# Optimization experiments

Hardware: AMD Instinct MI355X
Metric: run time of the kernel (lower is better)

Reference implementation:

```python
import jax, jax.numpy as jnp
import numpy as np

B, S, E, H = 2, 2048, 1024, 16
HD = E // H


def setup_inputs() -> dict:
    key = jax.random.key(0)
    ks = jax.random.split(key, 5)
    scale = 1.0 / np.sqrt(E)
    return {
        "x": jax.random.normal(ks[0], (B, S, E), dtype=jnp.float32),
        "Wq": jax.random.normal(ks[1], (H, HD, E), dtype=jnp.float32) * scale,
        "Wk": jax.random.normal(ks[2], (H, HD, E), dtype=jnp.float32) * scale,
        "Wv": jax.random.normal(ks[3], (H, HD, E), dtype=jnp.float32) * scale,
        "Wo": jax.random.normal(ks[4], (E, E), dtype=jnp.float32) * scale,
    }


def reference(x, Wq, Wk, Wv, Wo):
    # Batched per-head projections: torch Linear y = x @ W.T, W: [head_dim, E]
    q = jnp.einsum("bse,hde->bshd", x, Wq)  # [B,S,H,HD]
    k = jnp.einsum("bse,hde->bshd", x, Wk)
    v = jnp.einsum("bse,hde->bshd", x, Wv)
    # Scaled dot-product attention; original scales by sqrt(head_dim)
    scores = jnp.einsum("bqhd,bkhd->bhqk", q, k) / jnp.sqrt(jnp.float32(HD))
    attn = jax.nn.softmax(scores, axis=-1)  # [B,H,S,S]
    out_h = jnp.einsum("bhqk,bkhd->bqhd", attn, v)  # [B,S,H,HD]
    out_cat = out_h.reshape(x.shape[0], x.shape[1], -1)  # concat heads -> [B,S,E]
    return out_cat @ Wo.T
```

## Files before the change

### kernel.cpp

```cpp
#include <hip/hip_runtime.h>
#include <hip/hip_bf16.h>

typedef unsigned short u16;
typedef unsigned int u32;
typedef __attribute__((ext_vector_type(4))) float f32x4;
typedef __attribute__((ext_vector_type(16))) float f32x16;
typedef __attribute__((ext_vector_type(8))) short short8;
typedef __attribute__((ext_vector_type(8))) unsigned short u16x8;
typedef __attribute__((ext_vector_type(4))) unsigned short u16x4;
typedef __attribute__((ext_vector_type(4))) unsigned int u32x4;

#define BATCH 2
#define SEQ   2048
#define EMB   1024
#define NH    16
#define HD    64

__device__ inline u16 f2bf(float f) {
    unsigned u = __builtin_bit_cast(unsigned, f);
    unsigned r = u + 0x7FFFu + ((u >> 16) & 1u);
    return (u16)(r >> 16);
}

__device__ inline float fexp2(float x) {
    float r;
    asm("v_exp_f32 %0, %1" : "=v"(r) : "v"(x));
    return r;
}

__device__ inline void gload16(const void* g, void* l) {
    __builtin_amdgcn_global_load_lds(
        (const __attribute__((address_space(1))) unsigned int*)g,
        (__attribute__((address_space(3))) unsigned int*)l, 16, 0, 0);
}

__device__ inline short8 mk8(u32 a, u32 b, u32 c, u32 d) {
    u32x4 t; t[0] = a; t[1] = b; t[2] = c; t[3] = d;
    return __builtin_bit_cast(short8, t);
}

#define PACK_ST(st, w0,w1,w2,w3,w4,w5,w6,w7)                                   \
  {                                                                            \
    asm("v_cvt_pk_bf16_f32 %0, %1, %2" : "=v"(w0) : "v"(st[0]),  "v"(st[1]));  \
    asm("v_cvt_pk_bf16_f32 %0, %1, %2" : "=v"(w1) : "v"(st[2]),  "v"(st[3]));  \
    asm("v_cvt_pk_bf16_f32 %0, %1, %2" : "=v"(w2) : "v"(st[4]),  "v"(st[5]));  \
    asm("v_cvt_pk_bf16_f32 %0, %1, %2" : "=v"(w3) : "v"(st[6]),  "v"(st[7]));  \
    asm("v_permlane32_swap_b32 %0, %1" : "+v"(w0), "+v"(w2));                  \
    asm("v_permlane32_swap_b32 %0, %1" : "+v"(w1), "+v"(w3));                  \
    asm("v_cvt_pk_bf16_f32 %0, %1, %2" : "=v"(w4) : "v"(st[8]),  "v"(st[9]));  \
    asm("v_cvt_pk_bf16_f32 %0, %1, %2" : "=v"(w5) : "v"(st[10]), "v"(st[11])); \
    asm("v_cvt_pk_bf16_f32 %0, %1, %2" : "=v"(w6) : "v"(st[12]), "v"(st[13])); \
    asm("v_cvt_pk_bf16_f32 %0, %1, %2" : "=v"(w7) : "v"(st[14]), "v"(st[15])); \
    asm("v_permlane32_swap_b32 %0, %1" : "+v"(w4), "+v"(w6));                  \
    asm("v_permlane32_swap_b32 %0, %1" : "+v"(w5), "+v"(w7));                  \
  }

__global__ __launch_bounds__(256) void convert_all(
    const float* __restrict__ x,
    const float* __restrict__ Wq, const float* __restrict__ Wk, const float* __restrict__ Wv,
    u16* __restrict__ Xb, u16* __restrict__ Wqkv)
{
    const long gidx = (long)blockIdx.x * 2048 + (long)threadIdx.x * 8;
    const float* src;
    u16* dst;
    if (gidx < 4194304L) {
        src = x + gidx; dst = Xb + gidx;
    } else {
        const long r = gidx - 4194304L;
        const int w = (int)(r >> 20);
        const long off = r & 1048575L;
        src = (w == 0 ? Wq : w == 1 ? Wk : Wv) + off;
        dst = Wqkv + r;
    }
    f32x4 a = *(const f32x4*)src;
    f32x4 b = *(const f32x4*)(src + 4);
    u16x8 o;
    #pragma unroll
    for (int j = 0; j < 4; ++j) { o[j] = f2bf(a[j]); o[4 + j] = f2bf(b[j]); }
    *(u16x8*)dst = o;
}

__global__ __launch_bounds__(256) void convert_wo(
    const float* __restrict__ Wo, u16* __restrict__ Wob)
{
    const long gidx = (long)blockIdx.x * 2048 + (long)threadIdx.x * 8;
    f32x4 a = *(const f32x4*)(Wo + gidx);
    f32x4 b = *(const f32x4*)(Wo + gidx + 4);
    u16x8 o;
    #pragma unroll
    for (int j = 0; j < 4; ++j) { o[j] = f2bf(a[j]); o[4 + j] = f2bf(b[j]); }
    *(u16x8*)(Wob + gidx) = o;
}

__global__ __launch_bounds__(512, 2) void gemm256(
    const u16* __restrict__ A, const u16* __restrict__ Bb,
    u16* __restrict__ Qo, u16* __restrict__ Ko, u16* __restrict__ VTo)
{
    __shared__ u16 As[2][256 * 64];
    __shared__ u16 Bs[2][192 * 64];

    const int tid = threadIdx.x;
    const int lane = tid & 63;
    const int wid = tid >> 6;
    const int lr = lane & 15;
    const int lg = lane >> 4;
    const int wr = wid >> 2;
    const int wc = wid & 3;

    const int lin = blockIdx.y * 16 + blockIdx.x;
    const int swz = (lin & 7) * 32 + (lin >> 3);
    const int m0 = (swz & 15) * 256;
    const int n0 = (swz >> 4) * 192;

    const int grow = lane >> 3;
    const int schunk = ((lane & 7) ^ grow) << 4;

    auto issueTile = [&](int kt, int buf) {
        const int k0b = kt * 128;
        #pragma unroll
        for (int i = 0; i < 4; ++i) {
            const int row = i * 64 + wid * 8 + grow;
            gload16((const char*)A + (size_t)(m0 + row) * 2048 + k0b + schunk,
                    (char*)As[buf] + i * 8192 + wid * 1024);
        }
        #pragma unroll
        for (int i = 0; i < 3; ++i) {
            const int row = i * 64 + wid * 8 + grow;
            gload16((const char*)Bb + (size_t)(n0 + row) * 2048 + k0b + schunk,
                    (char*)Bs[buf] + i * 8192 + wid * 1024);
        }
    };

    issueTile(0, 0);
    issueTile(1, 1);

    f32x4 acc[8][3] = {};
    const int rsw = (lr & 7);

    for (int t = 0; t < 16; ++t) {
        if (t < 15) { asm volatile("s_waitcnt vmcnt(7)" ::: "memory"); }
        else        { asm volatile("s_waitcnt vmcnt(0)" ::: "memory"); }
        __builtin_amdgcn_sched_barrier(0);
        __builtin_amdgcn_s_barrier();
        __builtin_amdgcn_sched_barrier(0);

        const u16* Ac = As[t & 1];
        const u16* Bc = Bs[t & 1];

        short8 a[4][2], b[3][2];

        #pragma unroll
        for (int fi = 0; fi < 4; ++fi)
            #pragma unroll
            for (int ks = 0; ks < 2; ++ks)
                a[fi][ks] = *(const short8*)((const char*)Ac + (wr * 128 + fi * 16 + lr) * 128
                                             + (((ks * 4 + lg) ^ rsw) << 4));
        #pragma unroll
        for (int fj = 0; fj < 3; ++fj)
            #pragma unroll
            for (int ks = 0; ks < 2; ++ks)
                b[fj][ks] = *(const short8*)((const char*)Bc + (wc * 48 + fj * 16 + lr) * 128
                                             + (((ks * 4 + lg) ^ rsw) << 4));
        __builtin_amdgcn_s_setprio(1);
        #pragma unroll
        for (int fi = 0; fi < 4; ++fi)
            #pragma unroll
            for (int fj = 0; fj < 3; ++fj)
                #pragma unroll
                for (int ks = 0; ks < 2; ++ks)
                    acc[fi][fj] = __builtin_amdgcn_mfma_f32_16x16x32_bf16(a[fi][ks], b[fj][ks], acc[fi][fj], 0, 0, 0);
        __builtin_amdgcn_s_setprio(0);

        #pragma unroll
        for (int fi = 0; fi < 4; ++fi)
            #pragma unroll
            for (int ks = 0; ks < 2; ++ks)
                a[fi][ks] = *(const short8*)((const char*)Ac + (wr * 128 + (fi + 4) * 16 + lr) * 128
                                             + (((ks * 4 + lg) ^ rsw) << 4));
        __builtin_amdgcn_s_setprio(1);
        #pragma unroll
        for (int fi = 0; fi < 4; ++fi)
            #pragma unroll
            for (int fj = 0; fj < 3; ++fj)
                #pragma unroll
                for (int ks = 0; ks < 2; ++ks)
                    acc[fi + 4][fj] = __builtin_amdgcn_mfma_f32_16x16x32_bf16(a[fi][ks], b[fj][ks], acc[fi + 4][fj], 0, 0, 0);
        __builtin_amdgcn_s_setprio(0);

        __builtin_amdgcn_sched_barrier(0);
        __builtin_amdgcn_s_barrier();
        __builtin_amdgcn_sched_barrier(0);
        if (t + 2 < 16) issueTile(t + 2, t & 1);
    }

    const int mb = m0 + wr * 128;
    const int nb = n0 + wc * 48;
    #pragma unroll
    for (int fj = 0; fj < 3; ++fj) {
        const int nblk = nb + fj * 16;
        const int w = nblk >> 10;
        const float qs = (w == 0) ? 0.125f * 1.44269504f : 1.0f;
        const int nn = (nblk & 1023) + lr;
        const int h = nn >> 6, d = nn & 63;
        #pragma unroll
        for (int fi = 0; fi < 8; ++fi) {
            const int m = mb + fi * 16 + lg * 4;
            const int bb = m >> 11, s = m & 2047;
            const size_t bh = (size_t)(bb * NH + h);
            if (w == 2) {
                u16x4 v;
                #pragma unroll
                for (int i = 0; i < 4; ++i) v[i] = f2bf(acc[fi][fj][i]);
                *(u16x4*)&VTo[(bh * HD + d) * SEQ + s] = v;
            } else {
                u16* P = (w == 0) ? Qo : Ko;
                #pragma unroll
                for (int i = 0; i < 4; ++i)
                    P[(bh * SEQ + s + i) * HD + d] = f2bf(acc[fi][fj][i] * qs);
            }
        }
    }
}

__global__ __launch_bounds__(256) void gemm_out(
    const u16* __restrict__ A, const u16* __restrict__ Bb, float* __restrict__ Fo)
{
    __shared__ u16 As[2][128 * 64];
    __shared__ u16 Bs[2][128 * 64];

    const int tid = threadIdx.x;

    const int lin = blockIdx.y * 32 + blockIdx.x;
    const int swz = (lin & 7) * 32 + (lin >> 3);
    const int m0 = (swz & 31) * 128;
    const int n0 = (swz >> 5) * 128;

    const int lane = tid & 63;
    const int lr = lane & 15;
    const int lg = lane >> 4;
    const int wid = tid >> 6;
    const int wm = wid >> 1, wn = wid & 1;

    const int grow = lane >> 3;
    const int gcolb = ((lane & 7) ^ grow) << 4;
    const int rswz = (lr & 7);

    f32x4 acc[4][4] = {};

    auto issue = [&](int kt, int buf) {
        const int k0b = kt * 128;
        #pragma unroll
        for (int t = 0; t < 4; ++t) {
            const int row = (wid * 4 + t) * 8 + grow;
            gload16((const char*)A + (size_t)(m0 + row) * 2048 + k0b + gcolb,
                    (char*)As[buf] + (wid * 4 + t) * 1024);
            gload16((const char*)Bb + (size_t)(n0 + row) * 2048 + k0b + gcolb,
                    (char*)Bs[buf] + (wid * 4 + t) * 1024);
        }
    };

    issue(0, 0);
    issue(1, 1);

    for (int kt = 0; kt < 16; ++kt) {
        if (kt < 15) { asm volatile("s_waitcnt vmcnt(8)" ::: "memory"); }
        else         { asm volatile("s_waitcnt vmcnt(0)" ::: "memory"); }
        __builtin_amdgcn_sched_barrier(0);
        __builtin_amdgcn_s_barrier();
        __builtin_amdgcn_sched_barrier(0);

        const u16* Ac = As[kt & 1];
        const u16* Bc = Bs[kt & 1];
        #pragma unroll
        for (int kk = 0; kk < 2; ++kk) {
            short8 a[4], b[4];
            #pragma unroll
            for (int i = 0; i < 4; ++i)
                a[i] = *(const short8*)((const char*)Ac + (wm * 64 + i * 16 + lr) * 128
                                        + (((kk * 4 + lg) ^ rswz) << 4));
            #pragma unroll
            for (int i = 0; i < 4; ++i)
                b[i] = *(const short8*)((const char*)Bc + (wn * 64 + i * 16 + lr) * 128
                                        + (((kk * 4 + lg) ^ rswz) << 4));
            #pragma unroll
            for (int mi = 0; mi < 4; ++mi)
                #pragma unroll
                for (int ni = 0; ni < 4; ++ni)
                    acc[mi][ni] = __builtin_amdgcn_mfma_f32_16x16x32_bf16(a[mi], b[ni], acc[mi][ni], 0, 0, 0);
        }

        __builtin_amdgcn_sched_barrier(0);
        __builtin_amdgcn_s_barrier();
        __builtin_amdgcn_sched_barrier(0);
        if (kt + 2 < 16) issue(kt + 2, kt & 1);
    }

    const int mb = m0 + wm * 64;
    const int nb = n0 + wn * 64;
    #pragma unroll
    for (int mi = 0; mi < 4; ++mi)
        #pragma unroll
        for (int ni = 0; ni < 4; ++ni) {
            const int m = mb + mi * 16 + lg * 4;
            const int n = nb + ni * 16 + lr;
            #pragma unroll
            for (int i = 0; i < 4; ++i)
                Fo[(size_t)(m + i) * EMB + n] = acc[mi][ni][i];
        }
}

__global__ __launch_bounds__(256) void attn_fwd(
    const u16* __restrict__ Q, const u16* __restrict__ K,
    const u16* __restrict__ VT, u16* __restrict__ Cat)
{
    __shared__ u16 Ks[3][64 * 64];
    __shared__ u16 Vs[3][64 * 64];

    const int tid = threadIdx.x;
    const int lane = tid & 63;
    const int wid = tid >> 6;
    const int lq = lane & 31;
    const int hi = lane >> 5;

    const int lin = blockIdx.y * 16 + blockIdx.x;
    const int swz = (lin & 7) * 64 + (lin >> 3);
    const int qt = swz & 15;
    const int bh = swz >> 4;
    const int b = bh >> 4, h = bh & 15;

    const u16* Qg = Q + ((size_t)bh * SEQ + qt * 128 + wid * 32 + lq) * HD;
    short8 qf[4];
    #pragma unroll
    for (int ks = 0; ks < 4; ++ks)
        qf[ks] = *(const short8*)((const char*)Qg + ks * 32 + hi * 16);

    float lsum = 0.f;
    f32x16 ot0 = {}, ot1 = {};

    const u16* Kg = K + (size_t)bh * SEQ * HD;
    const u16* Vg = VT + (size_t)bh * HD * SEQ;

    const int srow = lane >> 3;
    const int schunk = ((lane & 7) ^ srow) << 4;

    auto issueKV = [&](int nt) {
        const int kv0 = nt * 64;
        const int slot = nt % 3;
        #pragma unroll
        for (int i = 0; i < 2; ++i) {
            const int krow = i * 32 + wid * 8 + srow;
            gload16((const char*)Kg + (size_t)(kv0 + krow) * 128 + schunk,
                    (char*)Ks[slot] + i * 4096 + wid * 1024);
            gload16((const char*)Vg + (size_t)krow * (SEQ * 2) + kv0 * 2 + schunk,
                    (char*)Vs[slot] + i * 4096 + wid * 1024);
        }
    };

    const int rsw = (lq & 7);

    auto tile2 = [&](const u16* KbufA, const u16* VbufA,
                     const u16* KbufB, const u16* VbufB) {
        f32x16 sA0 = {}, sA1 = {}, sB0 = {}, sB1 = {};
        #pragma unroll
        for (int ks = 0; ks < 4; ++ks) {
            const int co = ((ks * 2 + hi) ^ rsw) << 4;
            const short8 kA0 = *(const short8*)((const char*)KbufA + lq * 128 + co);
            const short8 kA1 = *(const short8*)((const char*)KbufA + (32 + lq) * 128 + co);
            const short8 kB0 = *(const short8*)((const char*)KbufB + lq * 128 + co);
            const short8 kB1 = *(const short8*)((const char*)KbufB + (32 + lq) * 128 + co);
            sA0 = __builtin_amdgcn_mfma_f32_32x32x16_bf16(kA0, qf[ks], sA0, 0, 0, 0);
            sA1 = __builtin_amdgcn_mfma_f32_32x32x16_bf16(kA1, qf[ks], sA1, 0, 0, 0);
            sB0 = __builtin_amdgcn_mfma_f32_32x32x16_bf16(kB0, qf[ks], sB0, 0, 0, 0);
            sB1 = __builtin_amdgcn_mfma_f32_32x32x16_bf16(kB1, qf[ks], sB1, 0, 0, 0);
        }

        #pragma unroll
        for (int i = 0; i < 16; ++i) {
            sA0[i] = fexp2(sA0[i]);
            sA1[i] = fexp2(sA1[i]);
            sB0[i] = fexp2(sB0[i]);
            sB1[i] = fexp2(sB1[i]);
        }
        float t0 = 0.f, t1 = 0.f, t2 = 0.f, t3 = 0.f;
        #pragma unroll
        for (int i = 0; i < 16; i += 4) {
            t0 += sA0[i]     + sA1[i]     + sB0[i]     + sB1[i];
            t1 += sA0[i + 1] + sA1[i + 1] + sB0[i + 1] + sB1[i + 1];
            t2 += sA0[i + 2] + sA1[i + 2] + sB0[i + 2] + sB1[i + 2];
            t3 += sA0[i + 3] + sA1[i + 3] + sB0[i + 3] + sB1[i + 3];
        }
        lsum += (t0 + t1) + (t2 + t3);

        u32 a0, a1, a2, a3, a4, a5, a6, a7;
        u32 c0, c1, c2, c3, c4, c5, c6, c7;
        PACK_ST(sA0, a0, a1, a2, a3, a4, a5, a6, a7);
        PACK_ST(sA1, c0, c1, c2, c3, c4, c5, c6, c7);
        const short8 pA0 = mk8(a0, a1, a2, a3);
        const short8 pA1 = mk8(a4, a5, a6, a7);
        const short8 pA2 = mk8(c0, c1, c2, c3);
        const short8 pA3 = mk8(c4, c5, c6, c7);
        u32 d0, d1, d2, d3, d4, d5, d6, d7;
        u32 e0, e1, e2, e3, e4, e5, e6, e7;
        PACK_ST(sB0, d0, d1, d2, d3, d4, d5, d6, d7);
        PACK_ST(sB1, e0, e1, e2, e3, e4, e5, e6, e7);
        const short8 pB0 = mk8(d0, d1, d2, d3);
        const short8 pB1 = mk8(d4, d5, d6, d7);
        const short8 pB2 = mk8(e0, e1, e2, e3);
        const short8 pB3 = mk8(e4, e5, e6, e7);

        #pragma unroll
        for (int ks = 0; ks < 4; ++ks) {
            const short8 pf = (ks == 0) ? pA0 : (ks == 1) ? pA1 : (ks == 2) ? pA2 : pA3;
            const int co = ((ks * 2 + hi) ^ rsw) << 4;
            const short8 vf0 = *(const short8*)((const char*)VbufA + lq * 128 + co);
            const short8 vf1 = *(const short8*)((const char*)VbufA + (32 + lq) * 128 + co);
            ot0 = __builtin_amdgcn_mfma_f32_32x32x16_bf16(vf0, pf, ot0, 0, 0, 0);
            ot1 = __builtin_amdgcn_mfma_f32_32x32x16_bf16(vf1, pf, ot1, 0, 0, 0);
        }
        #pragma unroll
        for (int ks = 0; ks < 4; ++ks) {
            const short8 pf = (ks == 0) ? pB0 : (ks == 1) ? pB1 : (ks == 2) ? pB2 : pB3;
            const int co = ((ks * 2 + hi) ^ rsw) << 4;
            const short8 vf0 = *(const short8*)((const char*)VbufB + lq * 128 + co);
            const short8 vf1 = *(const short8*)((const char*)VbufB + (32 + lq) * 128 + co);
            ot0 = __builtin_amdgcn_mfma_f32_32x32x16_bf16(vf0, pf, ot0, 0, 0, 0);
            ot1 = __builtin_amdgcn_mfma_f32_32x32x16_bf16(vf1, pf, ot1, 0, 0, 0);
        }
    };

    issueKV(0); issueKV(1); issueKV(2);

    for (int p = 0; p < 16; ++p) {
        if (p < 15) { asm volatile("s_waitcnt vmcnt(4)" ::: "memory"); }
        else        { asm volatile("s_waitcnt vmcnt(0)" ::: "memory"); }
        __builtin_amdgcn_sched_barrier(0);
        __builtin_amdgcn_s_barrier();
        __builtin_amdgcn_sched_barrier(0);

        const int s0 = (2 * p) % 3;
        const int s1 = (2 * p + 1) % 3;
        tile2(Ks[s0], Vs[s0], Ks[s1], Vs[s1]);

        __builtin_amdgcn_sched_barrier(0);
        __builtin_amdgcn_s_barrier();
        __builtin_amdgcn_sched_barrier(0);
        const int t3 = 2 * p + 3;
        if (t3 < 32)     issueKV(t3);
        if (t3 + 1 < 32) issueKV(t3 + 1);
    }

    const float l = lsum + __shfl_xor(lsum, 32);
    const float invl = 1.f / l;
    const int qrow = qt * 128 + wid * 32 + lq;
    u16* ob = Cat + ((size_t)b * SEQ + qrow) * EMB + h * HD;
    #pragma unroll
    for (int g = 0; g < 4; ++g) {
        u16x4 o0, o1;
        #pragma unroll
        for (int i = 0; i < 4; ++i) {
            o0[i] = f2bf(ot0[g * 4 + i] * invl);
            o1[i] = f2bf(ot1[g * 4 + i] * invl);
        }
        *(u16x4*)&ob[g * 8 + hi * 4] = o0;
        *(u16x4*)&ob[32 + g * 8 + hi * 4] = o1;
    }
}

extern "C" void kernel_launch(void* const* d_in, const int* in_sizes, int n_in,
                              void* d_out, int out_size, void* d_ws, size_t ws_size,
                              hipStream_t stream) {
    const float* x  = (const float*)d_in[0];
    const float* Wq = (const float*)d_in[1];
    const float* Wk = (const float*)d_in[2];
    const float* Wv = (const float*)d_in[3];
    const float* Wo = (const float*)d_in[4];
    float* out = (float*)d_out;

    u16* Xb   = (u16*)d_out;
    u16* Wqkv = (u16*)d_out + (size_t)4 * 1048576;

    char* ws = (char*)d_ws;
    u16* Qb  = (u16*)(ws);
    u16* Kb  = (u16*)(ws + (size_t)8  * 1048576);
    u16* VTb = (u16*)(ws + (size_t)16 * 1048576);
    u16* Cat = (u16*)(ws + (size_t)24 * 1048576);
    u16* Wob = Qb;

    convert_all<<<3584, 256, 0, stream>>>(x, Wq, Wk, Wv, Xb, Wqkv);

    dim3 g1(16, 16);
    gemm256<<<g1, 512, 0, stream>>>(Xb, Wqkv, Qb, Kb, VTb);

    dim3 g2(SEQ / 128, BATCH * NH);
    attn_fwd<<<g2, 256, 0, stream>>>(Qb, Kb, VTb, Cat);

    convert_wo<<<512, 256, 0, stream>>>(Wo, Wob);
    dim3 g3(4096 / 128, 1024 / 128);
    gemm_out<<<g3, 256, 0, stream>>>(Cat, Wob, out);
}
```

Measured before the change: 116.6 us.

## Deepen attention KV pipeline to five stages and fold Wo conversion into first kernel

The attention kernel's shared-memory K/V ring grows from three to five slots. Each barrier-delimited iteration now processes four KV tiles instead of two, which halves the number of block barriers and keeps more tiles in flight. Separately, when the workspace is large enough, Wo is converted to bf16 by the initial convert kernel into its own workspace region, which removes one kernel launch. The larger LDS footprint (80KB) may reduce the number of blocks resident per CU.

```diff
diff --git a/kernel.cpp b/kernel.cpp
--- a/kernel.cpp
+++ b/kernel.cpp
@@ -58,19 +58,26 @@
 __global__ __launch_bounds__(256) void convert_all(
     const float* __restrict__ x,
     const float* __restrict__ Wq, const float* __restrict__ Wk, const float* __restrict__ Wv,
-    u16* __restrict__ Xb, u16* __restrict__ Wqkv)
+    const float* __restrict__ Wo,
+    u16* __restrict__ Xb, u16* __restrict__ Wqkv, u16* __restrict__ Wob)
 {
-    const long gidx = (long)blockIdx.x * 2048 + (long)threadIdx.x * 8;
+    const int bid = blockIdx.x;
     const float* src;
     u16* dst;
-    if (gidx < 4194304L) {
-        src = x + gidx; dst = Xb + gidx;
+    if (bid < 3584) {
+        const long gidx = (long)bid * 2048 + (long)threadIdx.x * 8;
+        if (gidx < 4194304L) {
+            src = x + gidx; dst = Xb + gidx;
+        } else {
+            const long r = gidx - 4194304L;
+            const int w = (int)(r >> 20);
+            const long off = r & 1048575L;
+            src = (w == 0 ? Wq : w == 1 ? Wk : Wv) + off;
+            dst = Wqkv + r;
+        }
     } else {
-        const long r = gidx - 4194304L;
-        const int w = (int)(r >> 20);
-        const long off = r & 1048575L;
-        src = (w == 0 ? Wq : w == 1 ? Wk : Wv) + off;
-        dst = Wqkv + r;
+        const long gidx = (long)(bid - 3584) * 2048 + (long)threadIdx.x * 8;
+        src = Wo + gidx; dst = Wob + gidx;
     }
     f32x4 a = *(const f32x4*)src;
     f32x4 b = *(const f32x4*)(src + 4);
@@ -313,8 +320,8 @@
     const u16* __restrict__ Q, const u16* __restrict__ K,
     const u16* __restrict__ VT, u16* __restrict__ Cat)
 {
-    __shared__ u16 Ks[3][64 * 64];
-    __shared__ u16 Vs[3][64 * 64];
+    __shared__ u16 Ks[5][64 * 64];
+    __shared__ u16 Vs[5][64 * 64];
 
     const int tid = threadIdx.x;
     const int lane = tid & 63;
@@ -345,7 +352,7 @@
 
     auto issueKV = [&](int nt) {
         const int kv0 = nt * 64;
-        const int slot = nt % 3;
+        const int slot = nt % 5;
         #pragma unroll
         for (int i = 0; i < 2; ++i) {
             const int krow = i * 32 + wid * 8 + srow;
@@ -428,25 +435,27 @@
         }
     };
 
-    issueKV(0); issueKV(1); issueKV(2);
-
-    for (int p = 0; p < 16; ++p) {
-        if (p < 15) { asm volatile("s_waitcnt vmcnt(4)" ::: "memory"); }
-        else        { asm volatile("s_waitcnt vmcnt(0)" ::: "memory"); }
+    issueKV(0); issueKV(1); issueKV(2); issueKV(3); issueKV(4);
+
+    for (int p = 0; p < 8; ++p) {
+        if (p < 7) { asm volatile("s_waitcnt vmcnt(4)" ::: "memory"); }
+        else       { asm volatile("s_waitcnt vmcnt(0)" ::: "memory"); }
         __builtin_amdgcn_sched_barrier(0);
         __builtin_amdgcn_s_barrier();
         __builtin_amdgcn_sched_barrier(0);
 
-        const int s0 = (2 * p) % 3;
-        const int s1 = (2 * p + 1) % 3;
-        tile2(Ks[s0], Vs[s0], Ks[s1], Vs[s1]);
+        const int t0 = 4 * p;
+        tile2(Ks[t0 % 5], Vs[t0 % 5], Ks[(t0 + 1) % 5], Vs[(t0 + 1) % 5]);
+        tile2(Ks[(t0 + 2) % 5], Vs[(t0 + 2) % 5], Ks[(t0 + 3) % 5], Vs[(t0 + 3) % 5]);
 
         __builtin_amdgcn_sched_barrier(0);
         __builtin_amdgcn_s_barrier();
         __builtin_amdgcn_sched_barrier(0);
-        const int t3 = 2 * p + 3;
-        if (t3 < 32)     issueKV(t3);
-        if (t3 + 1 < 32) issueKV(t3 + 1);
+        #pragma unroll
+        for (int j = 5; j <= 8; ++j) {
+            const int t = 4 * p + j;
+            if (t < 32) issueKV(t);
+        }
     }
 
     const float l = lsum + __shfl_xor(lsum, 32);
@@ -484,9 +493,12 @@
     u16* Kb  = (u16*)(ws + (size_t)8  * 1048576);
     u16* VTb = (u16*)(ws + (size_t)16 * 1048576);
     u16* Cat = (u16*)(ws + (size_t)24 * 1048576);
-    u16* Wob = Qb;
-
-    convert_all<<<3584, 256, 0, stream>>>(x, Wq, Wk, Wv, Xb, Wqkv);
+
+    const bool bigws = ws_size >= (size_t)34 * 1048576;
+    u16* Wob = bigws ? (u16*)(ws + (size_t)32 * 1048576) : Qb;
+
+    convert_all<<<bigws ? 4096 : 3584, 256, 0, stream>>>(x, Wq, Wk, Wv, Wo,
+                                                         Xb, Wqkv, Wob);
 
     dim3 g1(16, 16);
     gemm256<<<g1, 512, 0, stream>>>(Xb, Wqkv, Qb, Kb, VTb);
@@ -494,7 +506,7 @@
     dim3 g2(SEQ / 128, BATCH * NH);
     attn_fwd<<<g2, 256, 0, stream>>>(Qb, Kb, VTb, Cat);
 
-    convert_wo<<<512, 256, 0, stream>>>(Wo, Wob);
+    if (!bigws) convert_wo<<<512, 256, 0, stream>>>(Wo, Wob);
     dim3 g3(4096 / 128, 1024 / 128);
     gemm_out<<<g3, 256, 0, stream>>>(Cat, Wob, out);
 }
```

Result: slower. 125.6 us (+7.7%).
